# Optimization experiments

Measured on AMD Instinct MI355X. Metric: run time of the kernel, lower is better.

Reference implementation:

```python
import jax, jax.numpy as jnp
import numpy as np
import math

N, E = 50000, 800000
NFEAT, HID, NCLASS = 512, 96, 64
NUM_LAYERS = 8
ALPHA, THETA = 0.1, 0.5


def setup_inputs() -> dict:
    key = jax.random.key(0)
    ks = jax.random.split(key, 8)
    x = jax.random.normal(ks[0], (N, NFEAT), dtype=jnp.float32)
    # dense_to_sparse(adj_t) -> edge_index; weights are discarded by the module,
    # so propagation uses unit edge weights. We generate the edge list directly.
    edge_index = jax.random.randint(ks[1], (2, E), 0, N, dtype=jnp.int32)
    s_in = 1.0 / math.sqrt(NFEAT)
    s_hid = 1.0 / math.sqrt(HID)
    W_in = jax.random.uniform(ks[2], (NFEAT, HID), jnp.float32, -s_in, s_in)
    b_in = jax.random.uniform(ks[3], (HID,), jnp.float32, -s_in, s_in)
    conv_W = jax.random.uniform(ks[4], (NUM_LAYERS, HID, HID), jnp.float32, -s_hid, s_hid)
    W_out = jax.random.uniform(ks[5], (HID, NCLASS), jnp.float32, -s_hid, s_hid)
    b_out = jax.random.uniform(ks[6], (NCLASS,), jnp.float32, -s_hid, s_hid)
    return {"x": x, "edge_index": edge_index, "W_in": W_in, "b_in": b_in,
            "conv_W": conv_W, "W_out": W_out, "b_out": b_out}


def reference(x, edge_index, W_in, b_in, conv_W, W_out, b_out):
    # Eval mode: dropout is identity.
    src, dst = edge_index[0], edge_index[1]
    h = jax.nn.relu(x @ W_in + b_in)          # [N, HID]
    x0 = h
    for layer in range(NUM_LAYERS):
        beta = math.log(THETA / (layer + 1) + 1.0)
        # sparse propagation: out[i] = sum over edges (j -> i) of h[j]
        agg = jax.ops.segment_sum(h[src], dst, num_segments=N)   # [N, HID]
        hc = (1.0 - ALPHA) * agg + ALPHA * x0                    # initial residual
        h = jax.nn.relu((1.0 - beta) * hc + beta * (hc @ conv_W[layer]))
    out = h @ W_out + b_out                   # [N, NCLASS]
    return jax.nn.log_softmax(out, axis=-1)
```

## Files before the change

kernel.cpp:

```cpp
#include <hip/hip_runtime.h>
#include <math.h>

#define N_NODES 50000
#define N_EDGES 800000
#define NFEAT   512
#define HID     96
#define NCLASS  64
#define NUM_LAYERS 8
#define ALPHA   0.1f
#define NSB     49
#define NBB     196

typedef __attribute__((ext_vector_type(8))) short short8;
typedef __attribute__((ext_vector_type(4))) float f32x4;

__device__ __forceinline__ unsigned short f2bf(float f) {
    unsigned int u = __float_as_uint(f);
    unsigned int r = u + 0x7FFF + ((u >> 16) & 1);
    return (unsigned short)(r >> 16);
}
__device__ __forceinline__ float bflo(unsigned int u) { return __uint_as_float(u << 16); }
__device__ __forceinline__ float bfhi(unsigned int u) { return __uint_as_float(u & 0xFFFF0000u); }
__device__ __forceinline__ float bf2f(short s) {
    return __uint_as_float(((unsigned int)(unsigned short)s) << 16);
}

__device__ __forceinline__ void gload16(const float* g, float* l) {
    __builtin_amdgcn_global_load_lds(
        (const __attribute__((address_space(1))) void*)g,
        (__attribute__((address_space(3))) void*)l, 16, 0, 0);
}

__global__ void hist_kernel(const int* __restrict__ dst, int* __restrict__ deg) {
    int e = blockIdx.x * blockDim.x + threadIdx.x;
    if (e < N_EDGES) atomicAdd(&deg[dst[e]], 1);
}

__global__ void scan1_kernel(const int* __restrict__ deg, int* __restrict__ row_start,
                             int* __restrict__ blk_sum) {
    __shared__ int sd[1024];
    int t = threadIdx.x;
    int i = blockIdx.x * 1024 + t;
    int v = (i < N_NODES) ? ((deg[i] + 3) & ~3) : 0;
    sd[t] = v;
    __syncthreads();
    for (int off = 1; off < 1024; off <<= 1) {
        int tv = (t >= off) ? sd[t - off] : 0;
        __syncthreads();
        sd[t] += tv;
        __syncthreads();
    }
    if (i < N_NODES) row_start[i] = sd[t] - v;
    if (t == 1023) blk_sum[blockIdx.x] = sd[1023];
}

__global__ void scan2_kernel(const int* __restrict__ blk_sum, int* __restrict__ blk_off) {
    if (threadIdx.x == 0) {
        int acc = 0;
        for (int b = 0; b < NSB; b++) { blk_off[b] = acc; acc += blk_sum[b]; }
    }
}

__global__ void scan3_kernel(int* __restrict__ row_start, const int* __restrict__ blk_off) {
    int i = blockIdx.x * 1024 + threadIdx.x;
    if (i < N_NODES) row_start[i] += blk_off[blockIdx.x];
}

__global__ void fill_kernel(const int* __restrict__ src, const int* __restrict__ dst,
                            const int* __restrict__ row_start, int* __restrict__ cursor,
                            int* __restrict__ csr_src) {
    int e = blockIdx.x * blockDim.x + threadIdx.x;
    if (e < N_EDGES) {
        int d = dst[e];
        int pos = row_start[d] + atomicAdd(&cursor[d], 1);
        csr_src[pos] = src[e];
    }
}

__global__ void pad_kernel(const int* __restrict__ deg, const int* __restrict__ row_start,
                           int* __restrict__ csr_src) {
    int n = blockIdx.x * blockDim.x + threadIdx.x;
    if (n < N_NODES) {
        int d = deg[n], pd = (d + 3) & ~3, rs = row_start[n];
        for (int p = d; p < pd; p++) csr_src[rs + p] = N_NODES;
    }
}

__global__ __launch_bounds__(256) void bin_hist2_kernel(
        const int* __restrict__ deg, int* __restrict__ node_rank,
        int* __restrict__ blk_bin_cnt) {
    __shared__ int lh[64];
    int t = threadIdx.x;
    if (t < 64) lh[t] = 0;
    __syncthreads();
    int n = blockIdx.x * 256 + t;
    if (n < N_NODES) {
        int nq = (deg[n] + 3) >> 2; if (nq > 63) nq = 63;
        node_rank[n] = atomicAdd(&lh[nq], 1);
    }
    __syncthreads();
    if (t < 64) blk_bin_cnt[blockIdx.x * 64 + t] = lh[t];
}

__global__ void bin_offsets_kernel(const int* __restrict__ blk_bin_cnt,
                                   int* __restrict__ blk_bin_off,
                                   int* __restrict__ bin_base) {
    __shared__ int tot[64];
    int b = threadIdx.x;
    int acc = 0;
    for (int blk = 0; blk < NBB; blk++) {
        blk_bin_off[blk * 64 + b] = acc;
        acc += blk_bin_cnt[blk * 64 + b];
    }
    tot[b] = acc;
    __syncthreads();
    if (b == 0) {
        int a = 0;
        for (int i = 63; i >= 0; i--) { bin_base[i] = a; a += tot[i]; }
    }
}

__global__ __launch_bounds__(256) void bin_place_kernel(
        const int* __restrict__ deg, const int* __restrict__ node_rank,
        const int* __restrict__ blk_bin_off, const int* __restrict__ bin_base,
        int* __restrict__ perm) {
    int n = blockIdx.x * 256 + threadIdx.x;
    if (n < N_NODES) {
        int nq = (deg[n] + 3) >> 2; if (nq > 63) nq = 63;
        perm[bin_base[nq] + blk_bin_off[blockIdx.x * 64 + nq] + node_rank[n]] = n;
    }
}

__global__ void zero_dummy_kernel(short* __restrict__ h0, short* __restrict__ hb,
                                  short* __restrict__ hc) {
    int t = threadIdx.x;
    if (t < HID) {
        h0[(size_t)N_NODES * HID + t] = 0;
        hb[(size_t)N_NODES * HID + t] = 0;
        hc[(size_t)N_NODES * HID + t] = 0;
    }
}

__global__ void convert_win_kernel(const float* __restrict__ W, short* __restrict__ Wt) {
    int t = blockIdx.x * 256 + threadIdx.x;
    int lane = t & 63;
    int n    = (t >> 6) % 6;
    int ks   = t / 384;
    int quad = lane >> 4, l16 = lane & 15;
    short8 v;
#pragma unroll
    for (int j = 0; j < 8; j++)
        v[j] = (short)f2bf(W[(size_t)(ks * 32 + quad * 8 + j) * HID + n * 16 + l16]);
    *(short8*)&Wt[(size_t)t * 8] = v;
}

__global__ void convert_wout_kernel(const float* __restrict__ W, short* __restrict__ Wt) {
    int n = blockIdx.x;
    int k = threadIdx.x;
    Wt[(size_t)n * HID + k] = (short)f2bf(W[(size_t)k * NCLASS + n]);
}

__global__ void convert_wconv_kernel(const float* __restrict__ W, short* __restrict__ Wc) {
    int n = blockIdx.x;
    int l = blockIdx.y;
    int k = threadIdx.x;
    Wc[(size_t)l * HID * HID + (size_t)n * HID + k] =
        (short)f2bf(W[(size_t)l * HID * HID + (size_t)k * HID + n]);
}

__global__ __launch_bounds__(256) void gemm_in_kernel(
        const float* __restrict__ x, const short* __restrict__ WtT,
        const float* __restrict__ b, short* __restrict__ h0) {
    __shared__ __align__(16) float As[2][4096];
    int tid  = threadIdx.x;
    int wave = tid >> 6, lane = tid & 63;
    int quad = lane >> 4, l16 = lane & 15;
    int row0 = blockIdx.x * 64;

    const float* gsrc[4];
#pragma unroll
    for (int r = 0; r < 4; r++) {
        int rl  = r * 4 + (lane >> 4);
        int row = row0 + wave * 16 + rl;
        if (row >= N_NODES) row = N_NODES - 1;
        int c2s = (lane & 15) ^ rl;
        gsrc[r] = &x[(size_t)row * NFEAT + c2s * 4];
    }

    f32x4 acc[6];
#pragma unroll
    for (int n = 0; n < 6; n++) acc[n] = (f32x4){0.f, 0.f, 0.f, 0.f};

    {
        float* lb = &As[0][wave * 1024];
#pragma unroll
        for (int r = 0; r < 4; r++) gload16(gsrc[r], lb + r * 256);
    }

#pragma unroll
    for (int c = 0; c < 8; c++) {
        __syncthreads();
        if (c < 7) {
            float* nb = &As[(c + 1) & 1][wave * 1024];
#pragma unroll
            for (int r = 0; r < 4; r++) gload16(gsrc[r] + (c + 1) * 64, nb + r * 256);
        }
        const float* cb = &As[c & 1][wave * 1024 + l16 * 64];
#pragma unroll
        for (int s = 0; s < 2; s++) {
            int c2a = s * 8 + quad * 2;
            f32x4 fa = *(const f32x4*)&cb[((c2a    ) ^ l16) * 4];
            f32x4 fb = *(const f32x4*)&cb[((c2a + 1) ^ l16) * 4];
            union { short8 sv; uint4 u; } af;
            af.u.x = (unsigned)f2bf(fa[0]) | ((unsigned)f2bf(fa[1]) << 16);
            af.u.y = (unsigned)f2bf(fa[2]) | ((unsigned)f2bf(fa[3]) << 16);
            af.u.z = (unsigned)f2bf(fb[0]) | ((unsigned)f2bf(fb[1]) << 16);
            af.u.w = (unsigned)f2bf(fb[2]) | ((unsigned)f2bf(fb[3]) << 16);
            int ks = c * 2 + s;
            const short* bbase = &WtT[(size_t)(ks * 6) * 512 + lane * 8];
#pragma unroll
            for (int n = 0; n < 6; n++) {
                short8 bfrag = *(const short8*)&bbase[n * 512];
                acc[n] = __builtin_amdgcn_mfma_f32_16x16x32_bf16(af.sv, bfrag, acc[n], 0, 0, 0);
            }
        }
    }

    int row0w = row0 + wave * 16;
#pragma unroll
    for (int n = 0; n < 6; n++) {
        int col = n * 16 + l16;
        float bias = b[col];
#pragma unroll
        for (int r = 0; r < 4; r++) {
            int grow = row0w + quad * 4 + r;
            if (grow < N_NODES) {
                float v = acc[n][r] + bias;
                v = v > 0.f ? v : 0.f;
                h0[(size_t)grow * HID + col] = (short)f2bf(v);
            }
        }
    }
}

__global__ __launch_bounds__(384) void layer_kernel(
        const short* __restrict__ h_in, const short* __restrict__ x0bf,
        const int* __restrict__ row_start, const int* __restrict__ deg,
        const int* __restrict__ csr_src, const int* __restrict__ perm,
        const short* __restrict__ Wc, float beta, short* __restrict__ h_out) {
    __shared__ short As[32][104];
    __shared__ int   snode[32];
    int tid = threadIdx.x;
    int tx = tid % 12;
    int ty = tid / 12;
    int idx = blockIdx.x * 32 + ty;
    bool valid = idx < N_NODES;
    int node = valid ? perm[idx] : (N_NODES - 1);
    if (tx == 0) snode[ty] = valid ? node : -1;

    int s = row_start[node];
    int d = deg[node];
    int nq = (d + 3) >> 2;
    const int4* c4 = (const int4*)(csr_src + s);
    float acc[8];
#pragma unroll
    for (int j = 0; j < 8; j++) acc[j] = 0.f;
    for (int i = 0; i < nq; i++) {
        int4 idxv = c4[i];
        uint4 a0 = *(const uint4*)&h_in[(size_t)idxv.x * HID + tx * 8];
        uint4 a1 = *(const uint4*)&h_in[(size_t)idxv.y * HID + tx * 8];
        uint4 a2 = *(const uint4*)&h_in[(size_t)idxv.z * HID + tx * 8];
        uint4 a3 = *(const uint4*)&h_in[(size_t)idxv.w * HID + tx * 8];
        acc[0] += bflo(a0.x) + bflo(a1.x) + bflo(a2.x) + bflo(a3.x);
        acc[1] += bfhi(a0.x) + bfhi(a1.x) + bfhi(a2.x) + bfhi(a3.x);
        acc[2] += bflo(a0.y) + bflo(a1.y) + bflo(a2.y) + bflo(a3.y);
        acc[3] += bfhi(a0.y) + bfhi(a1.y) + bfhi(a2.y) + bfhi(a3.y);
        acc[4] += bflo(a0.z) + bflo(a1.z) + bflo(a2.z) + bflo(a3.z);
        acc[5] += bfhi(a0.z) + bfhi(a1.z) + bfhi(a2.z) + bfhi(a3.z);
        acc[6] += bflo(a0.w) + bflo(a1.w) + bflo(a2.w) + bflo(a3.w);
        acc[7] += bfhi(a0.w) + bfhi(a1.w) + bfhi(a2.w) + bfhi(a3.w);
    }
    uint4 xq = *(const uint4*)&x0bf[(size_t)node * HID + tx * 8];
    float hc[8];
    hc[0] = (1.f - ALPHA) * acc[0] + ALPHA * bflo(xq.x);
    hc[1] = (1.f - ALPHA) * acc[1] + ALPHA * bfhi(xq.x);
    hc[2] = (1.f - ALPHA) * acc[2] + ALPHA * bflo(xq.y);
    hc[3] = (1.f - ALPHA) * acc[3] + ALPHA * bfhi(xq.y);
    hc[4] = (1.f - ALPHA) * acc[4] + ALPHA * bflo(xq.z);
    hc[5] = (1.f - ALPHA) * acc[5] + ALPHA * bfhi(xq.z);
    hc[6] = (1.f - ALPHA) * acc[6] + ALPHA * bflo(xq.w);
    hc[7] = (1.f - ALPHA) * acc[7] + ALPHA * bfhi(xq.w);
    {
        uint4 pk;
        pk.x = (unsigned)f2bf(hc[0]) | ((unsigned)f2bf(hc[1]) << 16);
        pk.y = (unsigned)f2bf(hc[2]) | ((unsigned)f2bf(hc[3]) << 16);
        pk.z = (unsigned)f2bf(hc[4]) | ((unsigned)f2bf(hc[5]) << 16);
        pk.w = (unsigned)f2bf(hc[6]) | ((unsigned)f2bf(hc[7]) << 16);
        *(uint4*)&As[ty][tx * 8] = pk;
    }
    __syncthreads();

    int wave = tid >> 6, lane = tid & 63;
    int quad = lane >> 4, l16 = lane & 15;
    int rt = wave & 1;
    int ct0 = (wave >> 1) * 2, ct1 = ct0 + 1;

    f32x4 g0 = (f32x4){0.f,0.f,0.f,0.f}, g1 = (f32x4){0.f,0.f,0.f,0.f};
#pragma unroll
    for (int ks = 0; ks < 3; ks++) {
        short8 afrag = *(const short8*)&As[rt * 16 + l16][ks * 32 + quad * 8];
        short8 b0 = *(const short8*)&Wc[(size_t)(ct0 * 16 + l16) * HID + ks * 32 + quad * 8];
        short8 b1 = *(const short8*)&Wc[(size_t)(ct1 * 16 + l16) * HID + ks * 32 + quad * 8];
        g0 = __builtin_amdgcn_mfma_f32_16x16x32_bf16(afrag, b0, g0, 0, 0, 0);
        g1 = __builtin_amdgcn_mfma_f32_16x16x32_bf16(afrag, b1, g1, 0, 0, 0);
    }
    float ob = 1.0f - beta;
#pragma unroll
    for (int r = 0; r < 4; r++) {
        int lrow = rt * 16 + quad * 4 + r;
        int nd = snode[lrow];
        if (nd >= 0) {
            int c0 = ct0 * 16 + l16;
            int c1 = ct1 * 16 + l16;
            float v0 = ob * bf2f(As[lrow][c0]) + beta * g0[r];
            float v1 = ob * bf2f(As[lrow][c1]) + beta * g1[r];
            v0 = v0 > 0.f ? v0 : 0.f;
            v1 = v1 > 0.f ? v1 : 0.f;
            h_out[(size_t)nd * HID + c0] = (short)f2bf(v0);
            h_out[(size_t)nd * HID + c1] = (short)f2bf(v1);
        }
    }
}

__global__ __launch_bounds__(256) void out_kernel(
        const short* __restrict__ h_bf, const short* __restrict__ Wt,
        const float* __restrict__ b, float* __restrict__ out) {
    int tid = threadIdx.x;
    int wave = tid >> 6, lane = tid & 63;
    int quad = lane >> 4, l16 = lane & 15;
    int row0 = blockIdx.x * 64 + wave * 16;

    f32x4 acc[4];
#pragma unroll
    for (int n = 0; n < 4; n++) acc[n] = (f32x4){0.f, 0.f, 0.f, 0.f};

    int arow = row0 + l16; if (arow > N_NODES) arow = N_NODES;
#pragma unroll
    for (int ks = 0; ks < 3; ks++) {
        short8 afrag = *(const short8*)&h_bf[(size_t)arow * HID + ks * 32 + quad * 8];
#pragma unroll
        for (int n = 0; n < 4; n++) {
            short8 bfrag = *(const short8*)&Wt[(size_t)(n * 16 + l16) * HID + ks * 32 + quad * 8];
            acc[n] = __builtin_amdgcn_mfma_f32_16x16x32_bf16(afrag, bfrag, acc[n], 0, 0, 0);
        }
    }
#pragma unroll
    for (int n = 0; n < 4; n++) {
        float bias = b[n * 16 + l16];
#pragma unroll
        for (int r = 0; r < 4; r++) acc[n][r] += bias;
    }
#pragma unroll
    for (int r = 0; r < 4; r++) {
        float m = acc[0][r];
        m = fmaxf(m, acc[1][r]); m = fmaxf(m, acc[2][r]); m = fmaxf(m, acc[3][r]);
#pragma unroll
        for (int off = 1; off < 16; off <<= 1) m = fmaxf(m, __shfl_xor(m, off));
        float s = __expf(acc[0][r] - m) + __expf(acc[1][r] - m)
                + __expf(acc[2][r] - m) + __expf(acc[3][r] - m);
#pragma unroll
        for (int off = 1; off < 16; off <<= 1) s += __shfl_xor(s, off);
        float lse = m + __logf(s);
        int grow = row0 + quad * 4 + r;
        if (grow < N_NODES) {
#pragma unroll
            for (int n = 0; n < 4; n++)
                out[(size_t)grow * NCLASS + n * 16 + l16] = acc[n][r] - lse;
        }
    }
}

extern "C" void kernel_launch(void* const* d_in, const int* in_sizes, int n_in,
                              void* d_out, int out_size, void* d_ws, size_t ws_size,
                              hipStream_t stream) {
    const float* x      = (const float*)d_in[0];
    const int*   ei     = (const int*)d_in[1];
    const int*   srcp   = ei;
    const int*   dstp   = ei + N_EDGES;
    const float* W_in   = (const float*)d_in[2];
    const float* b_in   = (const float*)d_in[3];
    const float* conv_W = (const float*)d_in[4];
    const float* W_out  = (const float*)d_in[5];
    const float* b_out  = (const float*)d_in[6];
    float* out = (float*)d_out;

    short* h0  = (short*)d_ws;
    short* h_b = h0  + (size_t)(N_NODES + 1) * HID;
    short* h_c = h_b + (size_t)(N_NODES + 1) * HID;
    short* Wt_in  = h_c + (size_t)(N_NODES + 1) * HID;
    short* Wt_out = Wt_in + (size_t)HID * NFEAT;
    short* Wc     = Wt_out + (size_t)NCLASS * HID;
    int* deg        = (int*)(Wc + (size_t)NUM_LAYERS * HID * HID);
    int* row_start  = deg + N_NODES;
    int* cursor     = row_start + N_NODES;
    int* blk_sum    = cursor + N_NODES;
    int* blk_off    = blk_sum + 64;
    int* bin_base   = blk_off + 64;
    int* node_rank  = bin_base + 64;
    int* perm       = node_rank + N_NODES;
    int* blk_bin_cnt= perm + N_NODES;
    int* blk_bin_off= blk_bin_cnt + NBB * 64;
    int* csr_src    = blk_bin_off + NBB * 64;

    hipMemsetAsync(deg,    0, N_NODES * sizeof(int), stream);
    hipMemsetAsync(cursor, 0, N_NODES * sizeof(int), stream);
    hist_kernel<<<(N_EDGES + 255) / 256, 256, 0, stream>>>(dstp, deg);
    scan1_kernel<<<NSB, 1024, 0, stream>>>(deg, row_start, blk_sum);
    scan2_kernel<<<1, 64, 0, stream>>>(blk_sum, blk_off);
    scan3_kernel<<<NSB, 1024, 0, stream>>>(row_start, blk_off);
    fill_kernel<<<(N_EDGES + 255) / 256, 256, 0, stream>>>(srcp, dstp, row_start, cursor, csr_src);
    pad_kernel<<<(N_NODES + 255) / 256, 256, 0, stream>>>(deg, row_start, csr_src);
    bin_hist2_kernel<<<NBB, 256, 0, stream>>>(deg, node_rank, blk_bin_cnt);
    bin_offsets_kernel<<<1, 64, 0, stream>>>(blk_bin_cnt, blk_bin_off, bin_base);
    bin_place_kernel<<<NBB, 256, 0, stream>>>(deg, node_rank, blk_bin_off, bin_base, perm);

    convert_win_kernel<<<24, 256, 0, stream>>>(W_in, Wt_in);
    convert_wout_kernel<<<NCLASS, HID, 0, stream>>>(W_out, Wt_out);
    convert_wconv_kernel<<<dim3(HID, NUM_LAYERS), HID, 0, stream>>>(conv_W, Wc);
    gemm_in_kernel<<<(N_NODES + 63) / 64, 256, 0, stream>>>(x, Wt_in, b_in, h0);
    zero_dummy_kernel<<<1, 128, 0, stream>>>(h0, h_b, h_c);

    short* cur = h0;
    short* nxt = h_b;
    for (int l = 0; l < NUM_LAYERS; l++) {
        float beta = logf(0.5f / (float)(l + 1) + 1.0f);
        layer_kernel<<<(N_NODES + 31) / 32, 384, 0, stream>>>(
            cur, h0, row_start, deg, csr_src, perm, Wc + (size_t)l * HID * HID, beta, nxt);
        cur = nxt;
        nxt = (cur == h_b) ? h_c : h_b;
    }

    out_kernel<<<(N_NODES + 63) / 64, 256, 0, stream>>>(cur, Wt_out, b_out, out);
}
```

Baseline: 538.1 us.

## Fuse eight GCNII layers into one persistent cooperative kernel with grid sync

Replaces the eight per-layer launches with a single cooperative persistent kernel that loops over 32-node tiles and uses grid.sync between layers, keeping the per-layer launch path as a fallback. It also merges the two small scan kernels by computing each block's offset with a wave shuffle reduction, prefetches the next CSR index quad in the gather loop, hoists the x0 load ahead of the loop, and stages outputs in LDS so each row is written with coalesced 16-byte stores. The aim is to remove launch gaps and tail effects between layers. The cost is grid-wide barriers, a fixed grid size limited by occupancy, and extra block syncs per tile.

```diff
diff --git a/kernel.cpp b/kernel.cpp
--- a/kernel.cpp
+++ b/kernel.cpp
@@ -1,5 +1,8 @@
 #include <hip/hip_runtime.h>
+#include <hip/hip_cooperative_groups.h>
 #include <math.h>
+
+namespace cg = cooperative_groups;
 
 #define N_NODES 50000
 #define N_EDGES 800000
@@ -10,6 +13,7 @@
 #define ALPHA   0.1f
 #define NSB     49
 #define NBB     196
+#define NT_TILES 1563
 
 typedef __attribute__((ext_vector_type(8))) short short8;
 typedef __attribute__((ext_vector_type(4))) float f32x4;
@@ -54,16 +58,18 @@
     if (t == 1023) blk_sum[blockIdx.x] = sd[1023];
 }
 
-__global__ void scan2_kernel(const int* __restrict__ blk_sum, int* __restrict__ blk_off) {
-    if (threadIdx.x == 0) {
-        int acc = 0;
-        for (int b = 0; b < NSB; b++) { blk_off[b] = acc; acc += blk_sum[b]; }
-    }
-}
-
-__global__ void scan3_kernel(int* __restrict__ row_start, const int* __restrict__ blk_off) {
-    int i = blockIdx.x * 1024 + threadIdx.x;
-    if (i < N_NODES) row_start[i] += blk_off[blockIdx.x];
+__global__ void scan3_kernel(int* __restrict__ row_start, const int* __restrict__ blk_sum) {
+    __shared__ int soff;
+    int t = threadIdx.x;
+    if (t < 64) {
+        int v = (t < blockIdx.x) ? blk_sum[t] : 0;
+#pragma unroll
+        for (int off = 1; off < 64; off <<= 1) v += __shfl_xor(v, off);
+        if (t == 0) soff = v;
+    }
+    __syncthreads();
+    int i = blockIdx.x * 1024 + t;
+    if (i < N_NODES) row_start[i] += soff;
 }
 
 __global__ void fill_kernel(const int* __restrict__ src, const int* __restrict__ dst,
@@ -243,17 +249,16 @@
     }
 }
 
-__global__ __launch_bounds__(384) void layer_kernel(
+__device__ __forceinline__ void layer_tile(
         const short* __restrict__ h_in, const short* __restrict__ x0bf,
         const int* __restrict__ row_start, const int* __restrict__ deg,
         const int* __restrict__ csr_src, const int* __restrict__ perm,
-        const short* __restrict__ Wc, float beta, short* __restrict__ h_out) {
-    __shared__ short As[32][104];
-    __shared__ int   snode[32];
+        const short* __restrict__ Wc, float beta, short* __restrict__ h_out,
+        int tile, short (*As)[104], int* snode) {
     int tid = threadIdx.x;
     int tx = tid % 12;
     int ty = tid / 12;
-    int idx = blockIdx.x * 32 + ty;
+    int idx = tile * 32 + ty;
     bool valid = idx < N_NODES;
     int node = valid ? perm[idx] : (N_NODES - 1);
     if (tx == 0) snode[ty] = valid ? node : -1;
@@ -262,11 +267,16 @@
     int d = deg[node];
     int nq = (d + 3) >> 2;
     const int4* c4 = (const int4*)(csr_src + s);
+    uint4 xq = *(const uint4*)&x0bf[(size_t)node * HID + tx * 8];
+
     float acc[8];
 #pragma unroll
     for (int j = 0; j < 8; j++) acc[j] = 0.f;
+    int4 nv = {0, 0, 0, 0};
+    if (nq > 0) nv = c4[0];
     for (int i = 0; i < nq; i++) {
-        int4 idxv = c4[i];
+        int4 idxv = nv;
+        if (i + 1 < nq) nv = c4[i + 1];
         uint4 a0 = *(const uint4*)&h_in[(size_t)idxv.x * HID + tx * 8];
         uint4 a1 = *(const uint4*)&h_in[(size_t)idxv.y * HID + tx * 8];
         uint4 a2 = *(const uint4*)&h_in[(size_t)idxv.z * HID + tx * 8];
@@ -280,7 +290,6 @@
         acc[6] += bflo(a0.w) + bflo(a1.w) + bflo(a2.w) + bflo(a3.w);
         acc[7] += bfhi(a0.w) + bfhi(a1.w) + bfhi(a2.w) + bfhi(a3.w);
     }
-    uint4 xq = *(const uint4*)&x0bf[(size_t)node * HID + tx * 8];
     float hc[8];
     hc[0] = (1.f - ALPHA) * acc[0] + ALPHA * bflo(xq.x);
     hc[1] = (1.f - ALPHA) * acc[1] + ALPHA * bfhi(xq.x);
@@ -315,21 +324,60 @@
         g1 = __builtin_amdgcn_mfma_f32_16x16x32_bf16(afrag, b1, g1, 0, 0, 0);
     }
     float ob = 1.0f - beta;
+    int c0 = ct0 * 16 + l16;
+    int c1 = ct1 * 16 + l16;
+    float v0s[4], v1s[4];
 #pragma unroll
     for (int r = 0; r < 4; r++) {
         int lrow = rt * 16 + quad * 4 + r;
-        int nd = snode[lrow];
-        if (nd >= 0) {
-            int c0 = ct0 * 16 + l16;
-            int c1 = ct1 * 16 + l16;
-            float v0 = ob * bf2f(As[lrow][c0]) + beta * g0[r];
-            float v1 = ob * bf2f(As[lrow][c1]) + beta * g1[r];
-            v0 = v0 > 0.f ? v0 : 0.f;
-            v1 = v1 > 0.f ? v1 : 0.f;
-            h_out[(size_t)nd * HID + c0] = (short)f2bf(v0);
-            h_out[(size_t)nd * HID + c1] = (short)f2bf(v1);
-        }
-    }
+        float v0 = ob * bf2f(As[lrow][c0]) + beta * g0[r];
+        float v1 = ob * bf2f(As[lrow][c1]) + beta * g1[r];
+        v0s[r] = v0 > 0.f ? v0 : 0.f;
+        v1s[r] = v1 > 0.f ? v1 : 0.f;
+    }
+    __syncthreads();
+#pragma unroll
+    for (int r = 0; r < 4; r++) {
+        int lrow = rt * 16 + quad * 4 + r;
+        As[lrow][c0] = (short)f2bf(v0s[r]);
+        As[lrow][c1] = (short)f2bf(v1s[r]);
+    }
+    __syncthreads();
+    int sn = snode[ty];
+    if (sn >= 0)
+        *(uint4*)&h_out[(size_t)sn * HID + tx * 8] = *(const uint4*)&As[ty][tx * 8];
+    __syncthreads();
+}
+
+__global__ __launch_bounds__(384) void coop_layers_kernel(
+        const short* __restrict__ h0, short* __restrict__ hb, short* __restrict__ hc,
+        const int* __restrict__ row_start, const int* __restrict__ deg,
+        const int* __restrict__ csr_src, const int* __restrict__ perm,
+        const short* __restrict__ Wc_all) {
+    __shared__ short As[32][104];
+    __shared__ int   snode[32];
+    cg::grid_group grid = cg::this_grid();
+    for (int l = 0; l < NUM_LAYERS; l++) {
+        const short* in = (l == 0) ? h0 : ((l & 1) ? hb : hc);
+        short* out = (l & 1) ? hc : hb;
+        float beta = logf(0.5f / (float)(l + 1) + 1.0f);
+        const short* Wc = Wc_all + (size_t)l * HID * HID;
+        for (int t = blockIdx.x; t < NT_TILES; t += gridDim.x)
+            layer_tile(in, h0, row_start, deg, csr_src, perm, Wc, beta, out, t, As, snode);
+        __threadfence();
+        grid.sync();
+    }
+}
+
+__global__ __launch_bounds__(384) void layer_kernel(
+        const short* __restrict__ h_in, const short* __restrict__ x0bf,
+        const int* __restrict__ row_start, const int* __restrict__ deg,
+        const int* __restrict__ csr_src, const int* __restrict__ perm,
+        const short* __restrict__ Wc, float beta, short* __restrict__ h_out) {
+    __shared__ short As[32][104];
+    __shared__ int   snode[32];
+    layer_tile(h_in, x0bf, row_start, deg, csr_src, perm, Wc, beta, h_out,
+               blockIdx.x, As, snode);
 }
 
 __global__ __launch_bounds__(256) void out_kernel(
@@ -404,8 +452,7 @@
     int* row_start  = deg + N_NODES;
     int* cursor     = row_start + N_NODES;
     int* blk_sum    = cursor + N_NODES;
-    int* blk_off    = blk_sum + 64;
-    int* bin_base   = blk_off + 64;
+    int* bin_base   = blk_sum + 64;
     int* node_rank  = bin_base + 64;
     int* perm       = node_rank + N_NODES;
     int* blk_bin_cnt= perm + N_NODES;
@@ -416,8 +463,7 @@
     hipMemsetAsync(cursor, 0, N_NODES * sizeof(int), stream);
     hist_kernel<<<(N_EDGES + 255) / 256, 256, 0, stream>>>(dstp, deg);
     scan1_kernel<<<NSB, 1024, 0, stream>>>(deg, row_start, blk_sum);
-    scan2_kernel<<<1, 64, 0, stream>>>(blk_sum, blk_off);
-    scan3_kernel<<<NSB, 1024, 0, stream>>>(row_start, blk_off);
+    scan3_kernel<<<NSB, 1024, 0, stream>>>(row_start, blk_sum);
     fill_kernel<<<(N_EDGES + 255) / 256, 256, 0, stream>>>(srcp, dstp, row_start, cursor, csr_src);
     pad_kernel<<<(N_NODES + 255) / 256, 256, 0, stream>>>(deg, row_start, csr_src);
     bin_hist2_kernel<<<NBB, 256, 0, stream>>>(deg, node_rank, blk_bin_cnt);
@@ -430,15 +476,32 @@
     gemm_in_kernel<<<(N_NODES + 63) / 64, 256, 0, stream>>>(x, Wt_in, b_in, h0);
     zero_dummy_kernel<<<1, 128, 0, stream>>>(h0, h_b, h_c);
 
-    short* cur = h0;
-    short* nxt = h_b;
-    for (int l = 0; l < NUM_LAYERS; l++) {
-        float beta = logf(0.5f / (float)(l + 1) + 1.0f);
-        layer_kernel<<<(N_NODES + 31) / 32, 384, 0, stream>>>(
-            cur, h0, row_start, deg, csr_src, perm, Wc + (size_t)l * HID * HID, beta, nxt);
-        cur = nxt;
-        nxt = (cur == h_b) ? h_c : h_b;
-    }
-
-    out_kernel<<<(N_NODES + 63) / 64, 256, 0, stream>>>(cur, Wt_out, b_out, out);
-}
+    bool coop_ok = false;
+    int nb = 0;
+    if (hipOccupancyMaxActiveBlocksPerMultiprocessor(
+            &nb, (const void*)coop_layers_kernel, 384, 0) == hipSuccess && nb > 0) {
+        int grid = nb * 256;
+        if (grid > NT_TILES) grid = NT_TILES;
+        const short* a_h0 = h0; short* a_hb = h_b; short* a_hc = h_c;
+        const int* a_rs = row_start; const int* a_deg = deg;
+        const int* a_csr = csr_src; const int* a_perm = perm;
+        const short* a_wc = Wc;
+        void* cargs[8] = {&a_h0, &a_hb, &a_hc, &a_rs, &a_deg, &a_csr, &a_perm, &a_wc};
+        if (hipLaunchCooperativeKernel((const void*)coop_layers_kernel,
+                dim3(grid), dim3(384), cargs, 0, stream) == hipSuccess)
+            coop_ok = true;
+    }
+    if (!coop_ok) {
+        short* cur = h0;
+        short* nxt = h_b;
+        for (int l = 0; l < NUM_LAYERS; l++) {
+            float beta = logf(0.5f / (float)(l + 1) + 1.0f);
+            layer_kernel<<<NT_TILES, 384, 0, stream>>>(
+                cur, h0, row_start, deg, csr_src, perm, Wc + (size_t)l * HID * HID, beta, nxt);
+            cur = nxt;
+            nxt = (cur == h_b) ? h_c : h_b;
+        }
+    }
+
+    out_kernel<<<(N_NODES + 63) / 64, 256, 0, stream>>>(h_c, Wt_out, b_out, out);
+}
```

New measurement: 1.137 ms. 2.11x slower.

## Process two node groups per layer block and stage outputs for coalesced stores

Applied to the files above, without the earlier changes.

The layer kernel now handles 64 nodes per block, with each thread gathering neighbours for two nodes in an interleaved loop to expose more memory-level parallelism. Each wave reuses the loaded weight fragments across two row tiles. Results are staged back through shared memory so each row is written with 16-byte vector stores instead of scattered 2-byte stores. The scan2 launch is merged into scan3 using a wave reduction. The cost is more registers per thread and half as many blocks, which may lower occupancy and worsen load balance where paired nodes differ in degree.

```diff
diff --git a/kernel.cpp b/kernel.cpp
--- a/kernel.cpp
+++ b/kernel.cpp
@@ -10,6 +10,7 @@
 #define ALPHA   0.1f
 #define NSB     49
 #define NBB     196
+#define NT64    782
 
 typedef __attribute__((ext_vector_type(8))) short short8;
 typedef __attribute__((ext_vector_type(4))) float f32x4;
@@ -54,16 +55,18 @@
     if (t == 1023) blk_sum[blockIdx.x] = sd[1023];
 }
 
-__global__ void scan2_kernel(const int* __restrict__ blk_sum, int* __restrict__ blk_off) {
-    if (threadIdx.x == 0) {
-        int acc = 0;
-        for (int b = 0; b < NSB; b++) { blk_off[b] = acc; acc += blk_sum[b]; }
-    }
-}
-
-__global__ void scan3_kernel(int* __restrict__ row_start, const int* __restrict__ blk_off) {
-    int i = blockIdx.x * 1024 + threadIdx.x;
-    if (i < N_NODES) row_start[i] += blk_off[blockIdx.x];
+__global__ void scan3_kernel(int* __restrict__ row_start, const int* __restrict__ blk_sum) {
+    __shared__ int soff;
+    int t = threadIdx.x;
+    if (t < 64) {
+        int v = (t < blockIdx.x) ? blk_sum[t] : 0;
+#pragma unroll
+        for (int off = 1; off < 64; off <<= 1) v += __shfl_xor(v, off);
+        if (t == 0) soff = v;
+    }
+    __syncthreads();
+    int i = blockIdx.x * 1024 + t;
+    if (i < N_NODES) row_start[i] += soff;
 }
 
 __global__ void fill_kernel(const int* __restrict__ src, const int* __restrict__ dst,
@@ -248,88 +251,146 @@
         const int* __restrict__ row_start, const int* __restrict__ deg,
         const int* __restrict__ csr_src, const int* __restrict__ perm,
         const short* __restrict__ Wc, float beta, short* __restrict__ h_out) {
-    __shared__ short As[32][104];
-    __shared__ int   snode[32];
+    __shared__ short As[64][104];
+    __shared__ int   snode[64];
     int tid = threadIdx.x;
     int tx = tid % 12;
     int ty = tid / 12;
-    int idx = blockIdx.x * 32 + ty;
-    bool valid = idx < N_NODES;
-    int node = valid ? perm[idx] : (N_NODES - 1);
-    if (tx == 0) snode[ty] = valid ? node : -1;
-
-    int s = row_start[node];
-    int d = deg[node];
-    int nq = (d + 3) >> 2;
-    const int4* c4 = (const int4*)(csr_src + s);
-    float acc[8];
-#pragma unroll
-    for (int j = 0; j < 8; j++) acc[j] = 0.f;
-    for (int i = 0; i < nq; i++) {
-        int4 idxv = c4[i];
-        uint4 a0 = *(const uint4*)&h_in[(size_t)idxv.x * HID + tx * 8];
-        uint4 a1 = *(const uint4*)&h_in[(size_t)idxv.y * HID + tx * 8];
-        uint4 a2 = *(const uint4*)&h_in[(size_t)idxv.z * HID + tx * 8];
-        uint4 a3 = *(const uint4*)&h_in[(size_t)idxv.w * HID + tx * 8];
-        acc[0] += bflo(a0.x) + bflo(a1.x) + bflo(a2.x) + bflo(a3.x);
-        acc[1] += bfhi(a0.x) + bfhi(a1.x) + bfhi(a2.x) + bfhi(a3.x);
-        acc[2] += bflo(a0.y) + bflo(a1.y) + bflo(a2.y) + bflo(a3.y);
-        acc[3] += bfhi(a0.y) + bfhi(a1.y) + bfhi(a2.y) + bfhi(a3.y);
-        acc[4] += bflo(a0.z) + bflo(a1.z) + bflo(a2.z) + bflo(a3.z);
-        acc[5] += bfhi(a0.z) + bfhi(a1.z) + bfhi(a2.z) + bfhi(a3.z);
-        acc[6] += bflo(a0.w) + bflo(a1.w) + bflo(a2.w) + bflo(a3.w);
-        acc[7] += bfhi(a0.w) + bfhi(a1.w) + bfhi(a2.w) + bfhi(a3.w);
-    }
-    uint4 xq = *(const uint4*)&x0bf[(size_t)node * HID + tx * 8];
-    float hc[8];
-    hc[0] = (1.f - ALPHA) * acc[0] + ALPHA * bflo(xq.x);
-    hc[1] = (1.f - ALPHA) * acc[1] + ALPHA * bfhi(xq.x);
-    hc[2] = (1.f - ALPHA) * acc[2] + ALPHA * bflo(xq.y);
-    hc[3] = (1.f - ALPHA) * acc[3] + ALPHA * bfhi(xq.y);
-    hc[4] = (1.f - ALPHA) * acc[4] + ALPHA * bflo(xq.z);
-    hc[5] = (1.f - ALPHA) * acc[5] + ALPHA * bfhi(xq.z);
-    hc[6] = (1.f - ALPHA) * acc[6] + ALPHA * bflo(xq.w);
-    hc[7] = (1.f - ALPHA) * acc[7] + ALPHA * bfhi(xq.w);
+    int idxA = blockIdx.x * 64 + ty;
+    int idxB = idxA + 32;
+    int nodeA = (idxA < N_NODES) ? perm[idxA] : (N_NODES - 1);
+    int nodeB = (idxB < N_NODES) ? perm[idxB] : (N_NODES - 1);
+    if (tx == 0) {
+        snode[ty]      = (idxA < N_NODES) ? nodeA : -1;
+        snode[ty + 32] = (idxB < N_NODES) ? nodeB : -1;
+    }
+
+    int sA = row_start[nodeA], sB = row_start[nodeB];
+    int nqA = (deg[nodeA] + 3) >> 2;
+    int nqB = (deg[nodeB] + 3) >> 2;
+    const int4* cA = (const int4*)(csr_src + sA);
+    const int4* cB = (const int4*)(csr_src + sB);
+    uint4 xqA = *(const uint4*)&x0bf[(size_t)nodeA * HID + tx * 8];
+    uint4 xqB = *(const uint4*)&x0bf[(size_t)nodeB * HID + tx * 8];
+
+    float accA[8], accB[8];
+#pragma unroll
+    for (int j = 0; j < 8; j++) { accA[j] = 0.f; accB[j] = 0.f; }
+    int nqm = nqA > nqB ? nqA : nqB;
+    const int4 dm4 = {N_NODES, N_NODES, N_NODES, N_NODES};
+#pragma unroll 2
+    for (int i = 0; i < nqm; i++) {
+        int4 ia = (i < nqA) ? cA[i] : dm4;
+        int4 ib = (i < nqB) ? cB[i] : dm4;
+        uint4 a0 = *(const uint4*)&h_in[(size_t)ia.x * HID + tx * 8];
+        uint4 a1 = *(const uint4*)&h_in[(size_t)ia.y * HID + tx * 8];
+        uint4 a2 = *(const uint4*)&h_in[(size_t)ia.z * HID + tx * 8];
+        uint4 a3 = *(const uint4*)&h_in[(size_t)ia.w * HID + tx * 8];
+        uint4 b0 = *(const uint4*)&h_in[(size_t)ib.x * HID + tx * 8];
+        uint4 b1 = *(const uint4*)&h_in[(size_t)ib.y * HID + tx * 8];
+        uint4 b2 = *(const uint4*)&h_in[(size_t)ib.z * HID + tx * 8];
+        uint4 b3 = *(const uint4*)&h_in[(size_t)ib.w * HID + tx * 8];
+        accA[0] += bflo(a0.x) + bflo(a1.x) + bflo(a2.x) + bflo(a3.x);
+        accA[1] += bfhi(a0.x) + bfhi(a1.x) + bfhi(a2.x) + bfhi(a3.x);
+        accA[2] += bflo(a0.y) + bflo(a1.y) + bflo(a2.y) + bflo(a3.y);
+        accA[3] += bfhi(a0.y) + bfhi(a1.y) + bfhi(a2.y) + bfhi(a3.y);
+        accA[4] += bflo(a0.z) + bflo(a1.z) + bflo(a2.z) + bflo(a3.z);
+        accA[5] += bfhi(a0.z) + bfhi(a1.z) + bfhi(a2.z) + bfhi(a3.z);
+        accA[6] += bflo(a0.w) + bflo(a1.w) + bflo(a2.w) + bflo(a3.w);
+        accA[7] += bfhi(a0.w) + bfhi(a1.w) + bfhi(a2.w) + bfhi(a3.w);
+        accB[0] += bflo(b0.x) + bflo(b1.x) + bflo(b2.x) + bflo(b3.x);
+        accB[1] += bfhi(b0.x) + bfhi(b1.x) + bfhi(b2.x) + bfhi(b3.x);
+        accB[2] += bflo(b0.y) + bflo(b1.y) + bflo(b2.y) + bflo(b3.y);
+        accB[3] += bfhi(b0.y) + bfhi(b1.y) + bfhi(b2.y) + bfhi(b3.y);
+        accB[4] += bflo(b0.z) + bflo(b1.z) + bflo(b2.z) + bflo(b3.z);
+        accB[5] += bfhi(b0.z) + bfhi(b1.z) + bfhi(b2.z) + bfhi(b3.z);
+        accB[6] += bflo(b0.w) + bflo(b1.w) + bflo(b2.w) + bflo(b3.w);
+        accB[7] += bfhi(b0.w) + bfhi(b1.w) + bfhi(b2.w) + bfhi(b3.w);
+    }
     {
+        float h0v, h1v, h2v, h3v, h4v, h5v, h6v, h7v;
+        h0v = (1.f - ALPHA) * accA[0] + ALPHA * bflo(xqA.x);
+        h1v = (1.f - ALPHA) * accA[1] + ALPHA * bfhi(xqA.x);
+        h2v = (1.f - ALPHA) * accA[2] + ALPHA * bflo(xqA.y);
+        h3v = (1.f - ALPHA) * accA[3] + ALPHA * bfhi(xqA.y);
+        h4v = (1.f - ALPHA) * accA[4] + ALPHA * bflo(xqA.z);
+        h5v = (1.f - ALPHA) * accA[5] + ALPHA * bfhi(xqA.z);
+        h6v = (1.f - ALPHA) * accA[6] + ALPHA * bflo(xqA.w);
+        h7v = (1.f - ALPHA) * accA[7] + ALPHA * bfhi(xqA.w);
         uint4 pk;
-        pk.x = (unsigned)f2bf(hc[0]) | ((unsigned)f2bf(hc[1]) << 16);
-        pk.y = (unsigned)f2bf(hc[2]) | ((unsigned)f2bf(hc[3]) << 16);
-        pk.z = (unsigned)f2bf(hc[4]) | ((unsigned)f2bf(hc[5]) << 16);
-        pk.w = (unsigned)f2bf(hc[6]) | ((unsigned)f2bf(hc[7]) << 16);
+        pk.x = (unsigned)f2bf(h0v) | ((unsigned)f2bf(h1v) << 16);
+        pk.y = (unsigned)f2bf(h2v) | ((unsigned)f2bf(h3v) << 16);
+        pk.z = (unsigned)f2bf(h4v) | ((unsigned)f2bf(h5v) << 16);
+        pk.w = (unsigned)f2bf(h6v) | ((unsigned)f2bf(h7v) << 16);
         *(uint4*)&As[ty][tx * 8] = pk;
+        h0v = (1.f - ALPHA) * accB[0] + ALPHA * bflo(xqB.x);
+        h1v = (1.f - ALPHA) * accB[1] + ALPHA * bfhi(xqB.x);
+        h2v = (1.f - ALPHA) * accB[2] + ALPHA * bflo(xqB.y);
+        h3v = (1.f - ALPHA) * accB[3] + ALPHA * bfhi(xqB.y);
+        h4v = (1.f - ALPHA) * accB[4] + ALPHA * bflo(xqB.z);
+        h5v = (1.f - ALPHA) * accB[5] + ALPHA * bfhi(xqB.z);
+        h6v = (1.f - ALPHA) * accB[6] + ALPHA * bflo(xqB.w);
+        h7v = (1.f - ALPHA) * accB[7] + ALPHA * bfhi(xqB.w);
+        pk.x = (unsigned)f2bf(h0v) | ((unsigned)f2bf(h1v) << 16);
+        pk.y = (unsigned)f2bf(h2v) | ((unsigned)f2bf(h3v) << 16);
+        pk.z = (unsigned)f2bf(h4v) | ((unsigned)f2bf(h5v) << 16);
+        pk.w = (unsigned)f2bf(h6v) | ((unsigned)f2bf(h7v) << 16);
+        *(uint4*)&As[ty + 32][tx * 8] = pk;
     }
     __syncthreads();
 
     int wave = tid >> 6, lane = tid & 63;
     int quad = lane >> 4, l16 = lane & 15;
-    int rt = wave & 1;
+    int rtA = wave & 1, rtB = rtA + 2;
     int ct0 = (wave >> 1) * 2, ct1 = ct0 + 1;
 
-    f32x4 g0 = (f32x4){0.f,0.f,0.f,0.f}, g1 = (f32x4){0.f,0.f,0.f,0.f};
+    f32x4 gA0 = (f32x4){0.f,0.f,0.f,0.f}, gA1 = (f32x4){0.f,0.f,0.f,0.f};
+    f32x4 gB0 = (f32x4){0.f,0.f,0.f,0.f}, gB1 = (f32x4){0.f,0.f,0.f,0.f};
 #pragma unroll
     for (int ks = 0; ks < 3; ks++) {
-        short8 afrag = *(const short8*)&As[rt * 16 + l16][ks * 32 + quad * 8];
-        short8 b0 = *(const short8*)&Wc[(size_t)(ct0 * 16 + l16) * HID + ks * 32 + quad * 8];
-        short8 b1 = *(const short8*)&Wc[(size_t)(ct1 * 16 + l16) * HID + ks * 32 + quad * 8];
-        g0 = __builtin_amdgcn_mfma_f32_16x16x32_bf16(afrag, b0, g0, 0, 0, 0);
-        g1 = __builtin_amdgcn_mfma_f32_16x16x32_bf16(afrag, b1, g1, 0, 0, 0);
+        short8 afA = *(const short8*)&As[rtA * 16 + l16][ks * 32 + quad * 8];
+        short8 afB = *(const short8*)&As[rtB * 16 + l16][ks * 32 + quad * 8];
+        short8 w0 = *(const short8*)&Wc[(size_t)(ct0 * 16 + l16) * HID + ks * 32 + quad * 8];
+        short8 w1 = *(const short8*)&Wc[(size_t)(ct1 * 16 + l16) * HID + ks * 32 + quad * 8];
+        gA0 = __builtin_amdgcn_mfma_f32_16x16x32_bf16(afA, w0, gA0, 0, 0, 0);
+        gA1 = __builtin_amdgcn_mfma_f32_16x16x32_bf16(afA, w1, gA1, 0, 0, 0);
+        gB0 = __builtin_amdgcn_mfma_f32_16x16x32_bf16(afB, w0, gB0, 0, 0, 0);
+        gB1 = __builtin_amdgcn_mfma_f32_16x16x32_bf16(afB, w1, gB1, 0, 0, 0);
     }
     float ob = 1.0f - beta;
+    int c0 = ct0 * 16 + l16;
+    int c1 = ct1 * 16 + l16;
+    float vA0[4], vA1[4], vB0[4], vB1[4];
 #pragma unroll
     for (int r = 0; r < 4; r++) {
-        int lrow = rt * 16 + quad * 4 + r;
-        int nd = snode[lrow];
-        if (nd >= 0) {
-            int c0 = ct0 * 16 + l16;
-            int c1 = ct1 * 16 + l16;
-            float v0 = ob * bf2f(As[lrow][c0]) + beta * g0[r];
-            float v1 = ob * bf2f(As[lrow][c1]) + beta * g1[r];
-            v0 = v0 > 0.f ? v0 : 0.f;
-            v1 = v1 > 0.f ? v1 : 0.f;
-            h_out[(size_t)nd * HID + c0] = (short)f2bf(v0);
-            h_out[(size_t)nd * HID + c1] = (short)f2bf(v1);
-        }
-    }
+        int rowA = rtA * 16 + quad * 4 + r;
+        int rowB = rtB * 16 + quad * 4 + r;
+        float a0 = ob * bf2f(As[rowA][c0]) + beta * gA0[r];
+        float a1 = ob * bf2f(As[rowA][c1]) + beta * gA1[r];
+        float b0 = ob * bf2f(As[rowB][c0]) + beta * gB0[r];
+        float b1 = ob * bf2f(As[rowB][c1]) + beta * gB1[r];
+        vA0[r] = a0 > 0.f ? a0 : 0.f;
+        vA1[r] = a1 > 0.f ? a1 : 0.f;
+        vB0[r] = b0 > 0.f ? b0 : 0.f;
+        vB1[r] = b1 > 0.f ? b1 : 0.f;
+    }
+    __syncthreads();
+#pragma unroll
+    for (int r = 0; r < 4; r++) {
+        int rowA = rtA * 16 + quad * 4 + r;
+        int rowB = rtB * 16 + quad * 4 + r;
+        As[rowA][c0] = (short)f2bf(vA0[r]);
+        As[rowA][c1] = (short)f2bf(vA1[r]);
+        As[rowB][c0] = (short)f2bf(vB0[r]);
+        As[rowB][c1] = (short)f2bf(vB1[r]);
+    }
+    __syncthreads();
+    int snA = snode[ty];
+    int snB = snode[ty + 32];
+    if (snA >= 0)
+        *(uint4*)&h_out[(size_t)snA * HID + tx * 8] = *(const uint4*)&As[ty][tx * 8];
+    if (snB >= 0)
+        *(uint4*)&h_out[(size_t)snB * HID + tx * 8] = *(const uint4*)&As[ty + 32][tx * 8];
 }
 
 __global__ __launch_bounds__(256) void out_kernel(
@@ -404,8 +465,7 @@
     int* row_start  = deg + N_NODES;
     int* cursor     = row_start + N_NODES;
     int* blk_sum    = cursor + N_NODES;
-    int* blk_off    = blk_sum + 64;
-    int* bin_base   = blk_off + 64;
+    int* bin_base   = blk_sum + 64;
     int* node_rank  = bin_base + 64;
     int* perm       = node_rank + N_NODES;
     int* blk_bin_cnt= perm + N_NODES;
@@ -416,8 +476,7 @@
     hipMemsetAsync(cursor, 0, N_NODES * sizeof(int), stream);
     hist_kernel<<<(N_EDGES + 255) / 256, 256, 0, stream>>>(dstp, deg);
     scan1_kernel<<<NSB, 1024, 0, stream>>>(deg, row_start, blk_sum);
-    scan2_kernel<<<1, 64, 0, stream>>>(blk_sum, blk_off);
-    scan3_kernel<<<NSB, 1024, 0, stream>>>(row_start, blk_off);
+    scan3_kernel<<<NSB, 1024, 0, stream>>>(row_start, blk_sum);
     fill_kernel<<<(N_EDGES + 255) / 256, 256, 0, stream>>>(srcp, dstp, row_start, cursor, csr_src);
     pad_kernel<<<(N_NODES + 255) / 256, 256, 0, stream>>>(deg, row_start, csr_src);
     bin_hist2_kernel<<<NBB, 256, 0, stream>>>(deg, node_rank, blk_bin_cnt);
@@ -434,7 +493,7 @@
     short* nxt = h_b;
     for (int l = 0; l < NUM_LAYERS; l++) {
         float beta = logf(0.5f / (float)(l + 1) + 1.0f);
-        layer_kernel<<<(N_NODES + 31) / 32, 384, 0, stream>>>(
+        layer_kernel<<<NT64, 384, 0, stream>>>(
             cur, h0, row_start, deg, csr_src, perm, Wc + (size_t)l * HID * HID, beta, nxt);
         cur = nxt;
         nxt = (cur == h_b) ? h_c : h_b;
```

New measurement: 579.0 us. 7.6% more time.
